# Performance work log

Hardware: AMD Instinct MI355X
Metric: run time of the kernel (lower is better)

Reference implementation:

```python
import jax, jax.numpy as jnp
import numpy as np

OUT, IN, GROUP = 11008, 4096, 64
NUM_GROUPS = IN // GROUP  # pad = 0 since IN % GROUP == 0


def setup_inputs() -> dict:
    key = jax.random.key(0)
    k_x, k_q, k_s, k_b = jax.random.split(key, 4)
    x = jax.random.normal(k_x, (4, 2048, IN), dtype=jnp.float32)
    # int4 symmetric codes in [-8, 7], stored as int8 like the torch buffer
    qweight = jax.random.randint(k_q, (OUT, NUM_GROUPS, GROUP), -8, 8).astype(jnp.int8)
    # positive per-group scales (amax/7 in the original), stored fp16
    scales = (jax.random.uniform(k_s, (OUT, NUM_GROUPS), dtype=jnp.float32) * 0.02 + 1e-3).astype(jnp.float16)
    bias = (jax.random.normal(k_b, (OUT,), dtype=jnp.float32) * 0.02).astype(jnp.float16)
    return {"x": x, "qweight": qweight, "scales": scales, "bias": bias}


def reference(x, qweight, scales, bias):
    # Fused dequant: w[o, g*GROUP + j] = q[o, g, j] * scales[o, g]
    w = (qweight.astype(jnp.float16) * scales[:, :, None]).reshape(OUT, IN)
    w = w.astype(x.dtype)  # original casts dequantized weight to x.dtype
    # F.linear(x, w, bias): y = x @ w.T + b  -> [B, S, OUT]
    return jnp.einsum('bsi,oi->bso', x, w) + bias.astype(x.dtype)
```

## Files before the change

kernel.cpp:

```cpp
#include <hip/hip_runtime.h>
#include <hip/hip_fp16.h>
#include <stdint.h>


#define M_DIM 8192
#define N_DIM 11008
#define K_DIM 4096
#define MT_TILES 32
#define NT_TILES 43
#define K_TILES 128
#define SLAB 8192

typedef short short8 __attribute__((ext_vector_type(8)));
typedef float floatx4 __attribute__((ext_vector_type(4)));

__device__ __forceinline__ unsigned short f2bf(float f) {
  union { float f; uint32_t u; } c; c.f = f;
  uint32_t u = c.u;
  return (unsigned short)((u + 0x7FFFu + ((u >> 16) & 1u)) >> 16);
}

__device__ __forceinline__ float load_sc(const void* p, size_t idx, bool is_f32) {
  if (is_f32) return ((const float*)p)[idx];
  return __half2float(((const __half*)p)[idx]);
}

__device__ __forceinline__ bool sniff_q_is_i32(const void* qv) {
  const int* w = (const int*)qv;
  bool ok = true;
  #pragma unroll
  for (int j = 0; j < 16; ++j) {
    int v = w[j];
    ok = ok && (v == (int)(signed char)(v & 0xFF));
  }
  return ok;
}
__device__ __forceinline__ bool sniff_s_is_f32(const void* sv) {
  const float* f = (const float*)sv;
  bool ok = true;
  #pragma unroll
  for (int j = 0; j < 8; ++j) {
    float v = f[j];
    ok = ok && (v > 4e-4f) && (v < 6e-2f);
  }
  return ok;
}

__device__ __forceinline__ void gload_lds16(const short* g, short* l) {
  __builtin_amdgcn_global_load_lds(
      (const __attribute__((address_space(1))) uint32_t*)g,
      (__attribute__((address_space(3))) uint32_t*)l, 16, 0, 0);
}

__global__ __launch_bounds__(256)
void prep_fused(const float* __restrict__ x, const void* __restrict__ qv,
                const void* __restrict__ sv,
                short* __restrict__ xh, short* __restrict__ wq) {
  const int tid = threadIdx.x;
  int b = blockIdx.x;

  if (b < NT_TILES * 256) {
    const bool q_is_i32 = sniff_q_is_i32(qv);
    const bool s_is_f32 = sniff_s_is_f32(sv);
    const int nt = b >> 8;
    const int rem = b & 255;
    const int kt = rem >> 1, half = rem & 1;
    const int r = half * 128 + (tid >> 1);
    const int s0 = (tid & 1) * 2;
    const int o = nt * 256 + r;
    const int k0 = kt * 32 + s0 * 8;

    const float s = load_sc(sv, (size_t)o * 64 + (kt >> 1), s_is_f32);

    int codes[16];
    if (q_is_i32) {
      const int* qq = (const int*)qv + (size_t)o * K_DIM + k0;
      #pragma unroll
      for (int j = 0; j < 4; ++j) {
        int4 t = ((const int4*)qq)[j];
        codes[j*4+0]=t.x; codes[j*4+1]=t.y; codes[j*4+2]=t.z; codes[j*4+3]=t.w;
      }
    } else {
      union { int4 v; int8_t c[16]; } u;
      u.v = *(const int4*)((const int8_t*)qv + (size_t)o * K_DIM + k0);
      #pragma unroll
      for (int j = 0; j < 16; ++j) codes[j] = (int)u.c[j];
    }

    short8 h0, h1;
    #pragma unroll
    for (int j = 0; j < 8; ++j) h0[j] = f2bf((float)codes[j] * s);
    #pragma unroll
    for (int j = 0; j < 8; ++j) h1[j] = f2bf((float)codes[8 + j] * s);

    const int w = (r >> 1) & 3;
    short* slab = wq + ((size_t)nt * K_TILES + kt) * SLAB;
    *(short8*)&slab[r * 32 + ((s0    ) ^ w) * 8] = h0;
    *(short8*)&slab[r * 32 + ((s0 + 1) ^ w) * 8] = h1;
  } else {
    b -= NT_TILES * 256;
    const int mt = b >> 8;
    const int rem = b & 255;
    const int kt = rem >> 1, half = rem & 1;
    const int r = half * 128 + (tid >> 1);
    const int s0 = (tid & 1) * 2;
    const int k0 = kt * 32 + s0 * 8;

    const float4* p = (const float4*)(x + (size_t)(mt * 256 + r) * K_DIM + k0);
    float4 f0 = p[0], f1 = p[1], f2 = p[2], f3 = p[3];
    short8 h0, h1;
    h0[0]=f2bf(f0.x); h0[1]=f2bf(f0.y); h0[2]=f2bf(f0.z); h0[3]=f2bf(f0.w);
    h0[4]=f2bf(f1.x); h0[5]=f2bf(f1.y); h0[6]=f2bf(f1.z); h0[7]=f2bf(f1.w);
    h1[0]=f2bf(f2.x); h1[1]=f2bf(f2.y); h1[2]=f2bf(f2.z); h1[3]=f2bf(f2.w);
    h1[4]=f2bf(f3.x); h1[5]=f2bf(f3.y); h1[6]=f2bf(f3.z); h1[7]=f2bf(f3.w);

    const int w = (r >> 1) & 3;
    short* slab = xh + ((size_t)mt * K_TILES + kt) * SLAB;
    *(short8*)&slab[r * 32 + ((s0    ) ^ w) * 8] = h0;
    *(short8*)&slab[r * 32 + ((s0 + 1) ^ w) * 8] = h1;
  }
}

__global__ __launch_bounds__(512)
void gemm8(const short* __restrict__ xh, const short* __restrict__ wq,
           const void* __restrict__ sv, const void* __restrict__ bv,
           float* __restrict__ C) {
  __shared__ __align__(16) short lds[4 * 2 * SLAB];

  const bool s_is_f32 = sniff_s_is_f32(sv);

  const int tid  = threadIdx.x;
  const int lane = tid & 63;
  const int wid  = tid >> 6;
  const int wm = wid >> 2, wn = wid & 3;
  const int lr = lane & 15, lk = lane >> 4;

  const int bid = blockIdx.x;
  const int xcd = bid & 7;
  const int seq = bid >> 3;
  const int nt  = seq >> 2;
  const int mt  = xcd * 4 + (seq & 3);

  const short* Aslab = xh + (size_t)mt * K_TILES * SLAB;
  const short* Bslab = wq + (size_t)nt * K_TILES * SLAB;

  const int swz8 = (lk ^ ((lr >> 1) & 3)) << 3;
  int aoff[8], boff[4];
  #pragma unroll
  for (int mi = 0; mi < 8; ++mi) aoff[mi] = (wm * 128 + mi * 16 + lr) * 32 + swz8;
  #pragma unroll
  for (int ni = 0; ni < 4; ++ni) boff[ni] = (wn * 64 + ni * 16 + lr) * 32 + swz8;

  floatx4 acc[8][4];
  #pragma unroll
  for (int i = 0; i < 8; ++i)
    #pragma unroll
    for (int j = 0; j < 4; ++j)
      acc[i][j] = (floatx4){0.f, 0.f, 0.f, 0.f};

  short8 fa[8], fb[4], ga[8], gb[4];

#define STAGE(t) do {                                                   \
    const short* gA_ = Aslab + (size_t)(t) * SLAB;                      \
    const short* gB_ = Bslab + (size_t)(t) * SLAB;                      \
    short* lA_ = &lds[((t) & 3) * (2 * SLAB)];                          \
    short* lB_ = lA_ + SLAB;                                            \
    gload_lds16(gA_ + tid * 8,        lA_ + tid * 8);                   \
    gload_lds16(gA_ + 4096 + tid * 8, lA_ + 4096 + tid * 8);            \
    gload_lds16(gB_ + tid * 8,        lB_ + tid * 8);                   \
    gload_lds16(gB_ + 4096 + tid * 8, lB_ + 4096 + tid * 8);            \
  } while (0)

#define LOADF(da, db, t) do {                                           \
    const short* lA_ = &lds[((t) & 3) * (2 * SLAB)];                    \
    const short* lB_ = lA_ + SLAB;                                      \
    _Pragma("unroll")                                                   \
    for (int mi = 0; mi < 8; ++mi) da[mi] = *(const short8*)&lA_[aoff[mi]]; \
    _Pragma("unroll")                                                   \
    for (int ni = 0; ni < 4; ++ni) db[ni] = *(const short8*)&lB_[boff[ni]]; \
  } while (0)

#define DOMFMA(sa, sb) do {                                             \
    __builtin_amdgcn_s_setprio(1);                                      \
    _Pragma("unroll")                                                   \
    for (int mi = 0; mi < 8; ++mi)                                      \
      _Pragma("unroll")                                                 \
      for (int ni = 0; ni < 4; ++ni)                                    \
        acc[mi][ni] = __builtin_amdgcn_mfma_f32_16x16x32_bf16(          \
            sa[mi], sb[ni], acc[mi][ni], 0, 0, 0);                      \
    __builtin_amdgcn_s_setprio(0);                                      \
  } while (0)

#define SBAR __builtin_amdgcn_sched_barrier(0)
#define VMCNT(n) do { asm volatile("s_waitcnt vmcnt(" #n ")"); SBAR; } while (0)
#define BARRIER do { SBAR; __builtin_amdgcn_s_barrier(); SBAR; } while (0)

  STAGE(0); STAGE(1); STAGE(2);
  VMCNT(8);
  BARRIER;
  LOADF(fa, fb, 0);

  for (int kt = 0; kt < 124; kt += 2) {
    VMCNT(4);
    BARRIER;
    STAGE(kt + 3);
    LOADF(ga, gb, kt + 1);
    DOMFMA(fa, fb);
    VMCNT(4);
    BARRIER;
    STAGE(kt + 4);
    LOADF(fa, fb, kt + 2);
    DOMFMA(ga, gb);
  }

  VMCNT(4);
  BARRIER;
  STAGE(127);
  LOADF(ga, gb, 125);
  DOMFMA(fa, fb);
  VMCNT(4);
  BARRIER;
  LOADF(fa, fb, 126);
  DOMFMA(ga, gb);
  VMCNT(0);
  BARRIER;
  LOADF(ga, gb, 127);
  DOMFMA(fa, fb);
  DOMFMA(ga, gb);

#undef STAGE
#undef LOADF
#undef DOMFMA
#undef SBAR
#undef VMCNT
#undef BARRIER

  #pragma unroll
  for (int ni = 0; ni < 4; ++ni) {
    const int col = nt * 256 + wn * 64 + ni * 16 + lr;
    const float bvf = load_sc(bv, (size_t)col, s_is_f32);
    #pragma unroll
    for (int mi = 0; mi < 8; ++mi) {
      const int rbase = mt * 256 + wm * 128 + mi * 16 + lk * 4;
      #pragma unroll
      for (int rr = 0; rr < 4; ++rr)
        C[(size_t)(rbase + rr) * N_DIM + col] = acc[mi][ni][rr] + bvf;
    }
  }
}

__global__ __launch_bounds__(256)
void gemm_fused(const float* __restrict__ x, const void* __restrict__ qv,
                const void* __restrict__ sv, const void* __restrict__ bv,
                float* __restrict__ C) {
  __shared__ __align__(16) short As[128 * 64];
  __shared__ __align__(16) short Bs[128 * 64];

  const bool q_is_i32 = sniff_q_is_i32(qv);
  const bool s_is_f32 = sniff_s_is_f32(sv);

  const int tid  = threadIdx.x;
  const int lane = tid & 63;
  const int wid  = tid >> 6;
  const int wm = wid >> 1, wn = wid & 1;
  const int lr = lane & 15, lk = lane >> 4;

  const int nwg = gridDim.x;
  const int cpx = nwg >> 3;
  const int bid = blockIdx.x;
  const int swz = (bid & 7) * cpx + (bid >> 3);
  const int per_g = 4 * 86;
  const int g = swz / per_g;
  const int r = swz - g * per_g;
  const int mt = (g << 2) + (r & 3);
  const int nt = r >> 2;

  const int row0 = mt * 128;
  const int col0 = nt * 128;

  floatx4 acc[4][4];
  #pragma unroll
  for (int i = 0; i < 4; ++i)
    #pragma unroll
    for (int j = 0; j < 4; ++j)
      acc[i][j] = (floatx4){0.f, 0.f, 0.f, 0.f};

  for (int kt = 0; kt < K_DIM / 64; ++kt) {
    const int k0 = kt * 64;
    #pragma unroll
    for (int i = 0; i < 4; ++i) {
      const int cid = i * 256 + tid;
      const int arow = cid >> 3, ac = (cid & 7) << 3;
      const float4* p = (const float4*)(x + (size_t)(row0 + arow) * K_DIM + k0 + ac);
      float4 a = p[0], b = p[1];
      short8 h;
      h[0]=f2bf(a.x); h[1]=f2bf(a.y); h[2]=f2bf(a.z); h[3]=f2bf(a.w);
      h[4]=f2bf(b.x); h[5]=f2bf(b.y); h[6]=f2bf(b.z); h[7]=f2bf(b.w);
      *(short8*)&As[arow * 64 + ac] = h;
    }
    #pragma unroll
    for (int i = 0; i < 2; ++i) {
      const int cid = i * 256 + tid;
      const int brow = cid >> 2, bc = (cid & 3) << 4;
      const float s = load_sc(sv, (size_t)(col0 + brow) * 64 + kt, s_is_f32);
      int codes[16];
      if (q_is_i32) {
        const int* qq = (const int*)qv + (size_t)(col0 + brow) * K_DIM + k0 + bc;
        #pragma unroll
        for (int j = 0; j < 4; ++j) {
          int4 t = ((const int4*)qq)[j];
          codes[j*4+0]=t.x; codes[j*4+1]=t.y; codes[j*4+2]=t.z; codes[j*4+3]=t.w;
        }
      } else {
        union { int4 v; int8_t c[16]; } u;
        u.v = *(const int4*)((const int8_t*)qv + (size_t)(col0 + brow) * K_DIM + k0 + bc);
        #pragma unroll
        for (int j = 0; j < 16; ++j) codes[j] = (int)u.c[j];
      }
      short8 h0, h1;
      #pragma unroll
      for (int j = 0; j < 8; ++j) h0[j] = f2bf((float)codes[j] * s);
      #pragma unroll
      for (int j = 0; j < 8; ++j) h1[j] = f2bf((float)codes[8 + j] * s);
      *(short8*)&Bs[brow * 64 + bc]     = h0;
      *(short8*)&Bs[brow * 64 + bc + 8] = h1;
    }
    __syncthreads();
    #pragma unroll
    for (int ks = 0; ks < 2; ++ks) {
      short8 a[4], b[4];
      #pragma unroll
      for (int mi = 0; mi < 4; ++mi)
        a[mi] = *(const short8*)&As[(wm * 64 + mi * 16 + lr) * 64 + ks * 32 + lk * 8];
      #pragma unroll
      for (int ni = 0; ni < 4; ++ni)
        b[ni] = *(const short8*)&Bs[(wn * 64 + ni * 16 + lr) * 64 + ks * 32 + lk * 8];
      #pragma unroll
      for (int mi = 0; mi < 4; ++mi)
        #pragma unroll
        for (int ni = 0; ni < 4; ++ni)
          acc[mi][ni] = __builtin_amdgcn_mfma_f32_16x16x32_bf16(
              a[mi], b[ni], acc[mi][ni], 0, 0, 0);
    }
    __syncthreads();
  }

  #pragma unroll
  for (int ni = 0; ni < 4; ++ni) {
    const int col = col0 + wn * 64 + ni * 16 + lr;
    const float bvf = load_sc(bv, (size_t)col, s_is_f32);
    #pragma unroll
    for (int mi = 0; mi < 4; ++mi) {
      const int rbase = row0 + wm * 64 + mi * 16 + lk * 4;
      #pragma unroll
      for (int rr = 0; rr < 4; ++rr)
        C[(size_t)(rbase + rr) * N_DIM + col] = acc[mi][ni][rr] + bvf;
    }
  }
}

extern "C" void kernel_launch(void* const* d_in, const int* in_sizes, int n_in,
                              void* d_out, int out_size, void* d_ws, size_t ws_size,
                              hipStream_t stream) {
  const float* x  = (const float*)d_in[0];
  const void*  q  = (const void*)d_in[1];
  const void*  sc = (const void*)d_in[2];
  const void*  bs = (const void*)d_in[3];
  float* y = (float*)d_out;
  (void)in_sizes; (void)n_in; (void)out_size;

  const size_t xh_bytes = (size_t)M_DIM * K_DIM * 2;
  const size_t wq_bytes = (size_t)N_DIM * K_DIM * 2;

  if (ws_size >= xh_bytes + wq_bytes) {
    short* xh = (short*)d_ws;
    short* wq = (short*)((char*)d_ws + xh_bytes);
    prep_fused<<<NT_TILES * 256 + MT_TILES * 256, dim3(256), 0, stream>>>(
        x, q, sc, xh, wq);
    gemm8<<<MT_TILES * NT_TILES, dim3(512), 0, stream>>>(xh, wq, sc, bs, y);
  } else {
    gemm_fused<<<(M_DIM / 128) * (N_DIM / 128), dim3(256), 0, stream>>>(x, q, sc, bs, y);
  }
}
```

Before: 760.4 us.

## Switch GEMM to 64-wide K tiles with quarter-split ping-pong pipeline

The prep kernel now lays out the bf16 activation and weight copies in 256x64 tiles with an 8-way XOR swizzle, one block per row. The GEMM main loop uses two 64-deep LDS buffers instead of four 32-deep ones. Each K tile's MFMA work is split into four quadrant phases, with LDS fragment reads, global-to-LDS staging and barriers interleaved between them. The aim is to halve the number of K iterations and overlap memory traffic with MFMA at finer granularity. The cost is many more block-wide barriers and explicit lgkmcnt waits per tile, which may stall waves.

```diff
diff --git a/kernel.cpp b/kernel.cpp
--- a/kernel.cpp
+++ b/kernel.cpp
@@ -8,8 +8,8 @@
 #define K_DIM 4096
 #define MT_TILES 32
 #define NT_TILES 43
-#define K_TILES 128
-#define SLAB 8192
+#define KT64 64
+#define TSLAB 16384
 
 typedef short short8 __attribute__((ext_vector_type(8)));
 typedef float floatx4 __attribute__((ext_vector_type(4)));
@@ -57,20 +57,18 @@
                 const void* __restrict__ sv,
                 short* __restrict__ xh, short* __restrict__ wq) {
   const int tid = threadIdx.x;
-  int b = blockIdx.x;
-
-  if (b < NT_TILES * 256) {
+  const int b = blockIdx.x;
+  const int ktile = tid >> 2;
+  const int s0 = (tid & 3) * 2;
+  const int k0 = ktile * 64 + s0 * 8;
+
+  if (b < N_DIM) {
     const bool q_is_i32 = sniff_q_is_i32(qv);
     const bool s_is_f32 = sniff_s_is_f32(sv);
-    const int nt = b >> 8;
-    const int rem = b & 255;
-    const int kt = rem >> 1, half = rem & 1;
-    const int r = half * 128 + (tid >> 1);
-    const int s0 = (tid & 1) * 2;
-    const int o = nt * 256 + r;
-    const int k0 = kt * 32 + s0 * 8;
-
-    const float s = load_sc(sv, (size_t)o * 64 + (kt >> 1), s_is_f32);
+    const int o = b;
+    const int nt = o >> 8, r = o & 255;
+
+    const float s = load_sc(sv, (size_t)o * 64 + ktile, s_is_f32);
 
     int codes[16];
     if (q_is_i32) {
@@ -93,20 +91,15 @@
     #pragma unroll
     for (int j = 0; j < 8; ++j) h1[j] = f2bf((float)codes[8 + j] * s);
 
-    const int w = (r >> 1) & 3;
-    short* slab = wq + ((size_t)nt * K_TILES + kt) * SLAB;
-    *(short8*)&slab[r * 32 + ((s0    ) ^ w) * 8] = h0;
-    *(short8*)&slab[r * 32 + ((s0 + 1) ^ w) * 8] = h1;
+    short* slab = wq + ((size_t)nt * KT64 + ktile) * TSLAB;
+    const int sl0 = s0 ^ (r & 7);
+    *(short8*)&slab[r * 64 + sl0 * 8]       = h0;
+    *(short8*)&slab[r * 64 + (sl0 ^ 1) * 8] = h1;
   } else {
-    b -= NT_TILES * 256;
-    const int mt = b >> 8;
-    const int rem = b & 255;
-    const int kt = rem >> 1, half = rem & 1;
-    const int r = half * 128 + (tid >> 1);
-    const int s0 = (tid & 1) * 2;
-    const int k0 = kt * 32 + s0 * 8;
-
-    const float4* p = (const float4*)(x + (size_t)(mt * 256 + r) * K_DIM + k0);
+    const int m = b - N_DIM;
+    const int mt = m >> 8, r = m & 255;
+
+    const float4* p = (const float4*)(x + (size_t)m * K_DIM + k0);
     float4 f0 = p[0], f1 = p[1], f2 = p[2], f3 = p[3];
     short8 h0, h1;
     h0[0]=f2bf(f0.x); h0[1]=f2bf(f0.y); h0[2]=f2bf(f0.z); h0[3]=f2bf(f0.w);
@@ -114,10 +107,10 @@
     h1[0]=f2bf(f2.x); h1[1]=f2bf(f2.y); h1[2]=f2bf(f2.z); h1[3]=f2bf(f2.w);
     h1[4]=f2bf(f3.x); h1[5]=f2bf(f3.y); h1[6]=f2bf(f3.z); h1[7]=f2bf(f3.w);
 
-    const int w = (r >> 1) & 3;
-    short* slab = xh + ((size_t)mt * K_TILES + kt) * SLAB;
-    *(short8*)&slab[r * 32 + ((s0    ) ^ w) * 8] = h0;
-    *(short8*)&slab[r * 32 + ((s0 + 1) ^ w) * 8] = h1;
+    short* slab = xh + ((size_t)mt * KT64 + ktile) * TSLAB;
+    const int sl0 = s0 ^ (r & 7);
+    *(short8*)&slab[r * 64 + sl0 * 8]       = h0;
+    *(short8*)&slab[r * 64 + (sl0 ^ 1) * 8] = h1;
   }
 }
 
@@ -125,7 +118,7 @@
 void gemm8(const short* __restrict__ xh, const short* __restrict__ wq,
            const void* __restrict__ sv, const void* __restrict__ bv,
            float* __restrict__ C) {
-  __shared__ __align__(16) short lds[4 * 2 * SLAB];
+  __shared__ __align__(16) short lds[2 * 2 * TSLAB];
 
   const bool s_is_f32 = sniff_s_is_f32(sv);
 
@@ -141,15 +134,12 @@
   const int nt  = seq >> 2;
   const int mt  = xcd * 4 + (seq & 3);
 
-  const short* Aslab = xh + (size_t)mt * K_TILES * SLAB;
-  const short* Bslab = wq + (size_t)nt * K_TILES * SLAB;
-
-  const int swz8 = (lk ^ ((lr >> 1) & 3)) << 3;
-  int aoff[8], boff[4];
-  #pragma unroll
-  for (int mi = 0; mi < 8; ++mi) aoff[mi] = (wm * 128 + mi * 16 + lr) * 32 + swz8;
-  #pragma unroll
-  for (int ni = 0; ni < 4; ++ni) boff[ni] = (wn * 64 + ni * 16 + lr) * 32 + swz8;
+  const short* Aslab = xh + (size_t)mt * (KT64 * TSLAB);
+  const short* Bslab = wq + (size_t)nt * (KT64 * TSLAB);
+
+  int sk[2];
+  sk[0] = (lk ^ (lr & 7)) * 8;
+  sk[1] = sk[0] ^ 32;
 
   floatx4 acc[8][4];
   #pragma unroll
@@ -158,93 +148,162 @@
     for (int j = 0; j < 4; ++j)
       acc[i][j] = (floatx4){0.f, 0.f, 0.f, 0.f};
 
-  short8 fa[8], fb[4], ga[8], gb[4];
-
-#define STAGE(t) do {                                                   \
-    const short* gA_ = Aslab + (size_t)(t) * SLAB;                      \
-    const short* gB_ = Bslab + (size_t)(t) * SLAB;                      \
-    short* lA_ = &lds[((t) & 3) * (2 * SLAB)];                          \
-    short* lB_ = lA_ + SLAB;                                            \
-    gload_lds16(gA_ + tid * 8,        lA_ + tid * 8);                   \
-    gload_lds16(gA_ + 4096 + tid * 8, lA_ + 4096 + tid * 8);            \
-    gload_lds16(gB_ + tid * 8,        lB_ + tid * 8);                   \
-    gload_lds16(gB_ + 4096 + tid * 8, lB_ + 4096 + tid * 8);            \
+  short8 a[2][4], b0[2][2], b1[2][2];
+
+#define SBAR __builtin_amdgcn_sched_barrier(0)
+#define VMCNT(n) do { asm volatile("s_waitcnt vmcnt(" #n ")"); SBAR; } while (0)
+#define LGKM0 do { asm volatile("s_waitcnt lgkmcnt(0)"); SBAR; } while (0)
+#define BARRIER do { SBAR; __builtin_amdgcn_s_barrier(); SBAR; } while (0)
+
+#define STAGE_A(t, h) do {                                              \
+    const short* g_ = Aslab + (size_t)(t) * TSLAB + (h) * 8192;         \
+    short* l_ = lds + ((t) & 1) * (2 * TSLAB) + (h) * 8192;             \
+    gload_lds16(g_ + tid * 8,        l_ + tid * 8);                     \
+    gload_lds16(g_ + 4096 + tid * 8, l_ + 4096 + tid * 8);              \
   } while (0)
 
-#define LOADF(da, db, t) do {                                           \
-    const short* lA_ = &lds[((t) & 3) * (2 * SLAB)];                    \
-    const short* lB_ = lA_ + SLAB;                                      \
+#define STAGE_B(t, h) do {                                              \
+    const short* g_ = Bslab + (size_t)(t) * TSLAB + (h) * 8192;         \
+    short* l_ = lds + ((t) & 1) * (2 * TSLAB) + TSLAB + (h) * 8192;     \
+    gload_lds16(g_ + tid * 8,        l_ + tid * 8);                     \
+    gload_lds16(g_ + 4096 + tid * 8, l_ + 4096 + tid * 8);              \
+  } while (0)
+
+#define READS_A(mh, t) do {                                             \
+    const short* lA_ = lds + ((t) & 1) * (2 * TSLAB);                   \
     _Pragma("unroll")                                                   \
-    for (int mi = 0; mi < 8; ++mi) da[mi] = *(const short8*)&lA_[aoff[mi]]; \
+    for (int ks = 0; ks < 2; ++ks)                                      \
+      _Pragma("unroll")                                                 \
+      for (int mi = 0; mi < 4; ++mi)                                    \
+        a[ks][mi] = *(const short8*)&lA_[                               \
+            (wm * 128 + (mh) * 64 + mi * 16 + lr) * 64 + sk[ks]];       \
+  } while (0)
+
+#define READS_B(dst, nh, t) do {                                        \
+    const short* lB_ = lds + ((t) & 1) * (2 * TSLAB) + TSLAB;           \
     _Pragma("unroll")                                                   \
-    for (int ni = 0; ni < 4; ++ni) db[ni] = *(const short8*)&lB_[boff[ni]]; \
+    for (int ks = 0; ks < 2; ++ks)                                      \
+      _Pragma("unroll")                                                 \
+      for (int ni = 0; ni < 2; ++ni)                                    \
+        dst[ks][ni] = *(const short8*)&lB_[                             \
+            (wn * 64 + (nh) * 32 + ni * 16 + lr) * 64 + sk[ks]];        \
   } while (0)
 
-#define DOMFMA(sa, sb) do {                                             \
+#define MFMA_Q(mh, nh, bs) do {                                         \
     __builtin_amdgcn_s_setprio(1);                                      \
     _Pragma("unroll")                                                   \
-    for (int mi = 0; mi < 8; ++mi)                                      \
+    for (int mi = 0; mi < 4; ++mi)                                      \
       _Pragma("unroll")                                                 \
-      for (int ni = 0; ni < 4; ++ni)                                    \
-        acc[mi][ni] = __builtin_amdgcn_mfma_f32_16x16x32_bf16(          \
-            sa[mi], sb[ni], acc[mi][ni], 0, 0, 0);                      \
+      for (int ni = 0; ni < 2; ++ni) {                                  \
+        acc[(mh)*4+mi][(nh)*2+ni] = __builtin_amdgcn_mfma_f32_16x16x32_bf16( \
+            a[0][mi], bs[0][ni], acc[(mh)*4+mi][(nh)*2+ni], 0, 0, 0);   \
+        acc[(mh)*4+mi][(nh)*2+ni] = __builtin_amdgcn_mfma_f32_16x16x32_bf16( \
+            a[1][mi], bs[1][ni], acc[(mh)*4+mi][(nh)*2+ni], 0, 0, 0);   \
+      }                                                                 \
     __builtin_amdgcn_s_setprio(0);                                      \
   } while (0)
 
-#define SBAR __builtin_amdgcn_sched_barrier(0)
-#define VMCNT(n) do { asm volatile("s_waitcnt vmcnt(" #n ")"); SBAR; } while (0)
-#define BARRIER do { SBAR; __builtin_amdgcn_s_barrier(); SBAR; } while (0)
-
-  STAGE(0); STAGE(1); STAGE(2);
-  VMCNT(8);
-  BARRIER;
-  LOADF(fa, fb, 0);
-
-  for (int kt = 0; kt < 124; kt += 2) {
+  STAGE_B(0, 0); STAGE_B(0, 1);
+  STAGE_A(0, 0); STAGE_A(0, 1);
+  STAGE_B(1, 0); STAGE_B(1, 1);
+  VMCNT(4);
+  BARRIER;
+
+  for (int t0 = 0; t0 < 62; t0 += 2) {
+    const int t1 = t0 + 1;
+    READS_A(0, t0); READS_B(b0, 0, t0);
+    STAGE_A(t0 + 1, 0);
+    BARRIER; LGKM0;
+    MFMA_Q(0, 0, b0);
+    BARRIER;
+    READS_B(b1, 1, t0);
+    STAGE_A(t0 + 1, 1);
+    BARRIER; LGKM0;
+    MFMA_Q(0, 1, b1);
+    BARRIER;
+    READS_A(1, t0);
+    STAGE_B(t0 + 2, 0);
+    BARRIER; LGKM0;
+    MFMA_Q(1, 1, b1);
+    BARRIER;
+    STAGE_B(t0 + 2, 1);
     VMCNT(4);
     BARRIER;
-    STAGE(kt + 3);
-    LOADF(ga, gb, kt + 1);
-    DOMFMA(fa, fb);
+    MFMA_Q(1, 0, b0);
+    BARRIER;
+    READS_A(0, t1); READS_B(b0, 0, t1);
+    STAGE_A(t0 + 2, 0);
+    BARRIER; LGKM0;
+    MFMA_Q(0, 0, b0);
+    BARRIER;
+    READS_B(b1, 1, t1);
+    STAGE_A(t0 + 2, 1);
+    BARRIER; LGKM0;
+    MFMA_Q(0, 1, b1);
+    BARRIER;
+    READS_A(1, t1);
+    STAGE_B(t0 + 3, 0);
+    BARRIER; LGKM0;
+    MFMA_Q(1, 1, b1);
+    BARRIER;
+    STAGE_B(t0 + 3, 1);
     VMCNT(4);
     BARRIER;
-    STAGE(kt + 4);
-    LOADF(fa, fb, kt + 2);
-    DOMFMA(ga, gb);
-  }
-
-  VMCNT(4);
-  BARRIER;
-  STAGE(127);
-  LOADF(ga, gb, 125);
-  DOMFMA(fa, fb);
-  VMCNT(4);
-  BARRIER;
-  LOADF(fa, fb, 126);
-  DOMFMA(ga, gb);
+    MFMA_Q(1, 0, b0);
+    BARRIER;
+  }
+
+  READS_A(0, 62); READS_B(b0, 0, 62);
+  STAGE_A(63, 0);
+  BARRIER; LGKM0;
+  MFMA_Q(0, 0, b0);
+  BARRIER;
+  READS_B(b1, 1, 62);
+  STAGE_A(63, 1);
+  BARRIER; LGKM0;
+  MFMA_Q(0, 1, b1);
+  BARRIER;
+  READS_A(1, 62);
+  BARRIER; LGKM0;
+  MFMA_Q(1, 1, b1);
+  BARRIER;
   VMCNT(0);
   BARRIER;
-  LOADF(ga, gb, 127);
-  DOMFMA(fa, fb);
-  DOMFMA(ga, gb);
-
-#undef STAGE
-#undef LOADF
-#undef DOMFMA
+  MFMA_Q(1, 0, b0);
+  BARRIER;
+  READS_A(0, 63); READS_B(b0, 0, 63);
+  BARRIER; LGKM0;
+  MFMA_Q(0, 0, b0);
+  BARRIER;
+  READS_B(b1, 1, 63);
+  BARRIER; LGKM0;
+  MFMA_Q(0, 1, b1);
+  BARRIER;
+  READS_A(1, 63);
+  BARRIER; LGKM0;
+  MFMA_Q(1, 1, b1);
+  MFMA_Q(1, 0, b0);
+
+#undef STAGE_A
+#undef STAGE_B
+#undef READS_A
+#undef READS_B
+#undef MFMA_Q
 #undef SBAR
 #undef VMCNT
+#undef LGKM0
 #undef BARRIER
 
   #pragma unroll
-  for (int ni = 0; ni < 4; ++ni) {
-    const int col = nt * 256 + wn * 64 + ni * 16 + lr;
+  for (int nc = 0; nc < 4; ++nc) {
+    const int col = nt * 256 + wn * 64 + nc * 16 + lr;
     const float bvf = load_sc(bv, (size_t)col, s_is_f32);
     #pragma unroll
-    for (int mi = 0; mi < 8; ++mi) {
-      const int rbase = mt * 256 + wm * 128 + mi * 16 + lk * 4;
+    for (int L = 0; L < 8; ++L) {
+      const int rbase = mt * 256 + wm * 128 + (L >> 2) * 64 + (L & 3) * 16 + lk * 4;
       #pragma unroll
       for (int rr = 0; rr < 4; ++rr)
-        C[(size_t)(rbase + rr) * N_DIM + col] = acc[mi][ni][rr] + bvf;
+        C[(size_t)(rbase + rr) * N_DIM + col] = acc[L][nc][rr] + bvf;
     }
   }
 }
@@ -375,8 +434,7 @@
   if (ws_size >= xh_bytes + wq_bytes) {
     short* xh = (short*)d_ws;
     short* wq = (short*)((char*)d_ws + xh_bytes);
-    prep_fused<<<NT_TILES * 256 + MT_TILES * 256, dim3(256), 0, stream>>>(
-        x, q, sc, xh, wq);
+    prep_fused<<<N_DIM + M_DIM, dim3(256), 0, stream>>>(x, q, sc, xh, wq);
     gemm8<<<MT_TILES * NT_TILES, dim3(512), 0, stream>>>(xh, wq, sc, bs, y);
   } else {
     gemm_fused<<<(M_DIM / 128) * (N_DIM / 128), dim3(256), 0, stream>>>(x, q, sc, bs, y);
```

New measurement: 752.2 us. About the same (-1.1%).

## Switch GEMM to 128x256 tiles with two 256-thread blocks per CU

Applied to the files above, without the earlier changes.

Replaces the 512-thread 256x256-tile GEMM, which uses a 4-stage LDS ring, with a 256-thread 128x256-tile kernel. The new kernel uses a 3-stage LDS ring and launch bounds that allow two blocks per CU. It also adds explicit lgkmcnt(0) waits before each barrier and remaps block indices so that A half-slabs come from the existing 256-row prepacked layout. The aim is to raise occupancy and hide latency across independent blocks. The cost is less data reuse per tile, hence more global and L2 traffic, plus shallower pipelining.

```diff
diff --git a/kernel.cpp b/kernel.cpp
--- a/kernel.cpp
+++ b/kernel.cpp
@@ -6,10 +6,11 @@
 #define M_DIM 8192
 #define N_DIM 11008
 #define K_DIM 4096
-#define MT_TILES 32
+#define MT_TILES 64
 #define NT_TILES 43
 #define K_TILES 128
 #define SLAB 8192
+#define RSTRIDE 12288
 
 typedef short short8 __attribute__((ext_vector_type(8)));
 typedef float floatx4 __attribute__((ext_vector_type(4)));
@@ -121,108 +122,117 @@
   }
 }
 
-__global__ __launch_bounds__(512)
-void gemm8(const short* __restrict__ xh, const short* __restrict__ wq,
+__global__ __launch_bounds__(256, 2)
+void gemm4(const short* __restrict__ xh, const short* __restrict__ wq,
            const void* __restrict__ sv, const void* __restrict__ bv,
            float* __restrict__ C) {
-  __shared__ __align__(16) short lds[4 * 2 * SLAB];
+  __shared__ __align__(16) short lds[3 * RSTRIDE];
 
   const bool s_is_f32 = sniff_s_is_f32(sv);
 
   const int tid  = threadIdx.x;
   const int lane = tid & 63;
   const int wid  = tid >> 6;
-  const int wm = wid >> 2, wn = wid & 3;
+  const int wm = wid >> 1, wn = wid & 1;
   const int lr = lane & 15, lk = lane >> 4;
 
   const int bid = blockIdx.x;
   const int xcd = bid & 7;
   const int seq = bid >> 3;
-  const int nt  = seq >> 2;
-  const int mt  = xcd * 4 + (seq & 3);
-
-  const short* Aslab = xh + (size_t)mt * K_TILES * SLAB;
-  const short* Bslab = wq + (size_t)nt * K_TILES * SLAB;
+  const int nt  = seq >> 3;
+  const int mt  = xcd * 8 + (seq & 7);
+
+  const short* Aslab = xh + (size_t)(mt >> 1) * (K_TILES * SLAB) + (mt & 1) * 4096;
+  const short* Bslab = wq + (size_t)nt * (K_TILES * SLAB);
 
   const int swz8 = (lk ^ ((lr >> 1) & 3)) << 3;
-  int aoff[8], boff[4];
-  #pragma unroll
-  for (int mi = 0; mi < 8; ++mi) aoff[mi] = (wm * 128 + mi * 16 + lr) * 32 + swz8;
-  #pragma unroll
-  for (int ni = 0; ni < 4; ++ni) boff[ni] = (wn * 64 + ni * 16 + lr) * 32 + swz8;
-
-  floatx4 acc[8][4];
-  #pragma unroll
-  for (int i = 0; i < 8; ++i)
-    #pragma unroll
-    for (int j = 0; j < 4; ++j)
+  int aoff[4], boff[8];
+  #pragma unroll
+  for (int mi = 0; mi < 4; ++mi) aoff[mi] = (wm * 64 + mi * 16 + lr) * 32 + swz8;
+  #pragma unroll
+  for (int ni = 0; ni < 8; ++ni) boff[ni] = (wn * 128 + ni * 16 + lr) * 32 + swz8;
+
+  floatx4 acc[4][8];
+  #pragma unroll
+  for (int i = 0; i < 4; ++i)
+    #pragma unroll
+    for (int j = 0; j < 8; ++j)
       acc[i][j] = (floatx4){0.f, 0.f, 0.f, 0.f};
 
-  short8 fa[8], fb[4], ga[8], gb[4];
+  short8 fa[4], fb[8], ga[4], gb[8];
+
+#define SBAR __builtin_amdgcn_sched_barrier(0)
+#define VMCNT(n) do { asm volatile("s_waitcnt vmcnt(" #n ")"); SBAR; } while (0)
+#define LGKM0 do { asm volatile("s_waitcnt lgkmcnt(0)"); SBAR; } while (0)
+#define BARRIER do { SBAR; __builtin_amdgcn_s_barrier(); SBAR; } while (0)
 
 #define STAGE(t) do {                                                   \
+    const int s_ = (t) % 3;                                             \
     const short* gA_ = Aslab + (size_t)(t) * SLAB;                      \
     const short* gB_ = Bslab + (size_t)(t) * SLAB;                      \
-    short* lA_ = &lds[((t) & 3) * (2 * SLAB)];                          \
-    short* lB_ = lA_ + SLAB;                                            \
+    short* lA_ = lds + s_ * RSTRIDE;                                    \
+    short* lB_ = lA_ + 4096;                                            \
     gload_lds16(gA_ + tid * 8,        lA_ + tid * 8);                   \
-    gload_lds16(gA_ + 4096 + tid * 8, lA_ + 4096 + tid * 8);            \
+    gload_lds16(gA_ + 2048 + tid * 8, lA_ + 2048 + tid * 8);            \
     gload_lds16(gB_ + tid * 8,        lB_ + tid * 8);                   \
+    gload_lds16(gB_ + 2048 + tid * 8, lB_ + 2048 + tid * 8);            \
     gload_lds16(gB_ + 4096 + tid * 8, lB_ + 4096 + tid * 8);            \
+    gload_lds16(gB_ + 6144 + tid * 8, lB_ + 6144 + tid * 8);            \
   } while (0)
 
 #define LOADF(da, db, t) do {                                           \
-    const short* lA_ = &lds[((t) & 3) * (2 * SLAB)];                    \
-    const short* lB_ = lA_ + SLAB;                                      \
+    const short* lA_ = lds + ((t) % 3) * RSTRIDE;                       \
+    const short* lB_ = lA_ + 4096;                                      \
     _Pragma("unroll")                                                   \
-    for (int mi = 0; mi < 8; ++mi) da[mi] = *(const short8*)&lA_[aoff[mi]]; \
+    for (int mi = 0; mi < 4; ++mi) da[mi] = *(const short8*)&lA_[aoff[mi]]; \
     _Pragma("unroll")                                                   \
-    for (int ni = 0; ni < 4; ++ni) db[ni] = *(const short8*)&lB_[boff[ni]]; \
+    for (int ni = 0; ni < 8; ++ni) db[ni] = *(const short8*)&lB_[boff[ni]]; \
   } while (0)
 
 #define DOMFMA(sa, sb) do {                                             \
     __builtin_amdgcn_s_setprio(1);                                      \
     _Pragma("unroll")                                                   \
-    for (int mi = 0; mi < 8; ++mi)                                      \
+    for (int mi = 0; mi < 4; ++mi)                                      \
       _Pragma("unroll")                                                 \
-      for (int ni = 0; ni < 4; ++ni)                                    \
+      for (int ni = 0; ni < 8; ++ni)                                    \
         acc[mi][ni] = __builtin_amdgcn_mfma_f32_16x16x32_bf16(          \
             sa[mi], sb[ni], acc[mi][ni], 0, 0, 0);                      \
     __builtin_amdgcn_s_setprio(0);                                      \
   } while (0)
 
-#define SBAR __builtin_amdgcn_sched_barrier(0)
-#define VMCNT(n) do { asm volatile("s_waitcnt vmcnt(" #n ")"); SBAR; } while (0)
-#define BARRIER do { SBAR; __builtin_amdgcn_s_barrier(); SBAR; } while (0)
-
   STAGE(0); STAGE(1); STAGE(2);
-  VMCNT(8);
+  VMCNT(12);
   BARRIER;
   LOADF(fa, fb, 0);
 
   for (int kt = 0; kt < 124; kt += 2) {
-    VMCNT(4);
+    VMCNT(6);
+    LGKM0;
     BARRIER;
     STAGE(kt + 3);
     LOADF(ga, gb, kt + 1);
     DOMFMA(fa, fb);
-    VMCNT(4);
+    VMCNT(6);
+    LGKM0;
     BARRIER;
     STAGE(kt + 4);
     LOADF(fa, fb, kt + 2);
     DOMFMA(ga, gb);
   }
 
-  VMCNT(4);
+  VMCNT(6);
+  LGKM0;
   BARRIER;
   STAGE(127);
   LOADF(ga, gb, 125);
   DOMFMA(fa, fb);
-  VMCNT(4);
+  VMCNT(6);
+  LGKM0;
   BARRIER;
   LOADF(fa, fb, 126);
   DOMFMA(ga, gb);
   VMCNT(0);
+  LGKM0;
   BARRIER;
   LOADF(ga, gb, 127);
   DOMFMA(fa, fb);
@@ -233,15 +243,16 @@
 #undef DOMFMA
 #undef SBAR
 #undef VMCNT
+#undef LGKM0
 #undef BARRIER
 
   #pragma unroll
-  for (int ni = 0; ni < 4; ++ni) {
-    const int col = nt * 256 + wn * 64 + ni * 16 + lr;
+  for (int ni = 0; ni < 8; ++ni) {
+    const int col = nt * 256 + wn * 128 + ni * 16 + lr;
     const float bvf = load_sc(bv, (size_t)col, s_is_f32);
     #pragma unroll
-    for (int mi = 0; mi < 8; ++mi) {
-      const int rbase = mt * 256 + wm * 128 + mi * 16 + lk * 4;
+    for (int mi = 0; mi < 4; ++mi) {
+      const int rbase = mt * 128 + wm * 64 + mi * 16 + lk * 4;
       #pragma unroll
       for (int rr = 0; rr < 4; ++rr)
         C[(size_t)(rbase + rr) * N_DIM + col] = acc[mi][ni][rr] + bvf;
@@ -375,9 +386,9 @@
   if (ws_size >= xh_bytes + wq_bytes) {
     short* xh = (short*)d_ws;
     short* wq = (short*)((char*)d_ws + xh_bytes);
-    prep_fused<<<NT_TILES * 256 + MT_TILES * 256, dim3(256), 0, stream>>>(
+    prep_fused<<<NT_TILES * 256 + (M_DIM / 256) * 256, dim3(256), 0, stream>>>(
         x, q, sc, xh, wq);
-    gemm8<<<MT_TILES * NT_TILES, dim3(512), 0, stream>>>(xh, wq, sc, bs, y);
+    gemm4<<<MT_TILES * NT_TILES, dim3(256), 0, stream>>>(xh, wq, sc, bs, y);
   } else {
     gemm_fused<<<(M_DIM / 128) * (N_DIM / 128), dim3(256), 0, stream>>>(x, q, sc, bs, y);
   }
```

Measured after the change: 751.4 us, median of 2. No clear change (-1.2%).
